# Kernel optimization log

Measured on AMD Instinct MI355X. Metric: run time of the kernel, lower is better.

## Reference

```python
import jax, jax.numpy as jnp
import numpy as np

D, B, T, d = 4, 512, 64, 256  # num_dof, batch, seq_length, per-dof state dim


def setup_inputs() -> dict:
    key = jax.random.key(0)
    ks = jax.random.split(key, 17)
    w = lambda k, s: jax.random.normal(k, s, dtype=jnp.float32) * 0.05
    return {
        "x": jax.random.normal(ks[0], (D, B, T, d), dtype=jnp.float32),
        "wu": w(ks[1], (D, 2 * d, d)), "wf": w(ks[2], (D, 2 * d, d)),
        "wo": w(ks[3], (D, 2 * d, d)), "wc": w(ks[4], (D, 2 * d, d)),
        "bu": w(ks[5], (D, d)), "bf": w(ks[6], (D, d)),
        "bo": w(ks[7], (D, d)), "bc": w(ks[8], (D, d)),
        "gwu": w(ks[9], (D, D * d, d)), "gwf": w(ks[10], (D, D * d, d)),
        "gwo": w(ks[11], (D, D * d, d)), "gwc": w(ks[12], (D, D * d, d)),
        "gbu": w(ks[13], (D, d)), "gbf": w(ks[14], (D, d)),
        "gbo": w(ks[15], (D, d)), "gbc": w(ks[16], (D, d)),
    }


def reference(x, wu, wf, wo, wc, bu, bf, bo, bc,
              gwu, gwf, gwo, gwc, gbu, gbf, gbo, gbc):
    # x: [D, B, T, d]  (dof-stacked inputs_list)
    nD, nB, nT, nd = x.shape
    h0 = jnp.zeros((nD, nB, nd), x.dtype)
    m0 = jnp.zeros((nD, nB, nd), x.dtype)
    xt = jnp.transpose(x, (2, 0, 1, 3))  # [T, D, B, d]

    def step(carry, x_t):
        h, m = carry  # each [D, B, d]
        # --- per-dof LSTM cell (dofs independent here) ---
        inp = jnp.concatenate([x_t, h], axis=-1)  # [D, B, 2d]
        gu = jax.nn.sigmoid(jnp.einsum('dbi,dij->dbj', inp, wu) + bu[:, None, :])
        gf = jax.nn.sigmoid(jnp.einsum('dbi,dij->dbj', inp, wf) + bf[:, None, :])
        go = jax.nn.sigmoid(jnp.einsum('dbi,dij->dbj', inp, wo) + bo[:, None, :])
        gc = jnp.tanh(jnp.einsum('dbi,dij->dbj', inp, wc) + bc[:, None, :])
        m = gf * m + gu * gc
        h = jnp.tanh(go * m)
        # --- grid coupling step: hgrid = concat over dofs ---
        hg = jnp.transpose(h, (1, 0, 2)).reshape(nB, nD * nd)  # [B, D*d]
        gu2 = jax.nn.sigmoid(jnp.einsum('bs,dsj->dbj', hg, gwu) + gbu[:, None, :])
        gf2 = jax.nn.sigmoid(jnp.einsum('bs,dsj->dbj', hg, gwf) + gbf[:, None, :])
        go2 = jax.nn.sigmoid(jnp.einsum('bs,dsj->dbj', hg, gwo) + gbo[:, None, :])
        gc2 = jnp.tanh(jnp.einsum('bs,dsj->dbj', hg, gwc) + gbc[:, None, :])
        m = gf2 * m + gu2 * gc2
        h = jnp.tanh(go2 * m)
        return (h, m), None

    (h, m), _ = jax.lax.scan(step, (h0, m0), xt)
    # stacked [2, D, B, d]: [0]=h_list, [1]=m_list (dof along axis 1)
    return jnp.stack([h, m])
```

## Files before the change

kernel.cpp:

```cpp
#include <hip/hip_runtime.h>
#include <math.h>

#define NDOF 4
#define NB   512
#define NT   64
#define ND   256
#define NS   1024

#define GRID 256

typedef __attribute__((ext_vector_type(8))) __bf16 bf16x8;
typedef __attribute__((ext_vector_type(4))) float  f32x4;

__device__ __forceinline__ void gll16(const void* g, void* l) {
    __builtin_amdgcn_global_load_lds(
        (const __attribute__((address_space(1))) unsigned int*)g,
        (__attribute__((address_space(3))) unsigned int*)l, 16, 0, 0);
}

__device__ __forceinline__ float sig_(float x) { return 1.0f / (1.0f + __expf(-x)); }
__device__ __forceinline__ float tanh_(float x) {
    float e = __expf(-2.0f * fabsf(x));
    float t = (1.0f - e) / (1.0f + e);
    return copysignf(t, x);
}

__device__ __forceinline__ void store16_dev(__bf16* p, bf16x8 v) {
    asm volatile("global_store_dwordx4 %0, %1, off sc0 sc1" :: "v"(p), "v"(v) : "memory");
}
__device__ __forceinline__ void store_flag(unsigned* p, unsigned v) {
    asm volatile("global_store_dword %0, %1, off sc0 sc1" :: "v"(p), "v"(v) : "memory");
}
__device__ __forceinline__ unsigned flag_load(const unsigned* p) {
    unsigned v;
    asm volatile("global_load_dword %0, %1, off sc0 sc1\n\ts_waitcnt vmcnt(0)"
                 : "=v"(v) : "v"(p) : "memory");
    return v;
}

__device__ __forceinline__ void waitv0() {
    asm volatile("s_waitcnt vmcnt(0)" ::: "memory");
    __builtin_amdgcn_sched_barrier(0);
}
__device__ __forceinline__ void waitv8() {
    asm volatile("s_waitcnt vmcnt(8)" ::: "memory");
    __builtin_amdgcn_sched_barrier(0);
}
__device__ __forceinline__ void waitv12() {
    asm volatile("s_waitcnt vmcnt(12)" ::: "memory");
    __builtin_amdgcn_sched_barrier(0);
}

__device__ __forceinline__ void block_bar() {
    __builtin_amdgcn_sched_barrier(0);
    asm volatile("s_waitcnt lgkmcnt(0)\n\ts_barrier" ::: "memory");
    __builtin_amdgcn_sched_barrier(0);
}

__device__ __forceinline__ void poll_flags(const unsigned* f, int nf, unsigned e, int lane) {
    unsigned spins = 0;
    for (;;) {
        unsigned v = e;
        if (lane < nf) v = flag_load(f + lane);
        if (__all(v >= e)) break;
        __builtin_amdgcn_s_sleep(1);
        if (++spins > (1u << 15)) break;
    }
}

struct Params {
    const __bf16* xbf;
    const __bf16* wT1;
    const __bf16* wT2;
    const float *b1u, *b1f, *b1o, *b1c;
    const float *b2u, *b2f, *b2o, *b2c;
    const __bf16* hInit;
    __bf16* ring;
    float*  out;
    unsigned* flags;
};

__device__ __forceinline__ void issueB(bf16x8* smem, const __bf16* wrow,
                                       int pair, int rot, int mask, int tid) {
    const int rowB = tid & 127;
    const int kgb  = (tid >> 7) & 1;
    const int bb = 2048 + (pair & 3) * 1024;
    const int k0 = ((pair + rot) & mask) * 64;
    #pragma unroll
    for (int i = 0; i < 4; ++i) {
        const int kg = kgb + 2 * i;
        gll16(wrow + k0 + kg * 8, &smem[bb + kg * 128 + rowB]);
    }
}
template<int XIT>
__device__ __forceinline__ void issueA(bf16x8* smem, const __bf16* ax,
                                       const __bf16* ah, int pair, int rot, int mask,
                                       int tid) {
    const int rowA = tid & 63;
    const int kga  = tid >> 6;
    const int bb = (pair & 3) * 512;
    const __bf16* base;
    if (XIT > 0 && pair < XIT) base = ax + (size_t)rowA * ND + pair * 64;
    else base = ah + (size_t)rowA * NS + (((pair + rot) & mask) * 64 - XIT * 64);
    #pragma unroll
    for (int i = 0; i < 2; ++i) {
        const int kg = kga + 4 * i;
        gll16(base + kg * 8, &smem[bb + kg * 64 + rowA]);
    }
}

template<int NIT, int XIT>
__device__ __forceinline__ void gemm_seg(bf16x8* smem,
    const __bf16* ax, const __bf16* ah, const __bf16* wrow, int rot,
    const unsigned* gateF, int gateN, unsigned gateE,
    f32x4 (&acc)[2][4], int lane, int wr, int ws, int tid)
{
    constexpr int NSEG = NIT / 2;
    #pragma unroll 1
    for (int s = 0; s < NSEG; ++s) {
        waitv0();
        block_bar();
        if (s == 1 && gateF != nullptr) {
            if (tid < 64) poll_flags(gateF, gateN, gateE, lane);
            block_bar();
        }
        if (s + 1 < NSEG) {
            issueB(smem, wrow, 2 * s + 2, rot, NIT - 1, tid);
            issueB(smem, wrow, 2 * s + 3, rot, NIT - 1, tid);
            issueA<XIT>(smem, ax, ah, 2 * s + 2, rot, NIT - 1, tid);
            issueA<XIT>(smem, ax, ah, 2 * s + 3, rot, NIT - 1, tid);
        }
        #pragma unroll
        for (int q = 0; q < 2; ++q) {
            const int bbA = ((2 * s + q) & 3) * 512;
            const int bbB = 2048 + ((2 * s + q) & 3) * 1024;
            #pragma unroll
            for (int sub = 0; sub < 2; ++sub) {
                const int kq = sub * 4 + (lane >> 4);
                bf16x8 a[2], b[4];
                #pragma unroll
                for (int mI = 0; mI < 2; ++mI)
                    a[mI] = smem[bbA + kq * 64 + wr + mI * 16 + (lane & 15)];
                #pragma unroll
                for (int g = 0; g < 4; ++g)
                    b[g] = smem[bbB + kq * 128 + g * 32 + ws * 16 + (lane & 15)];
                #pragma unroll
                for (int mI = 0; mI < 2; ++mI)
                    #pragma unroll
                    for (int g = 0; g < 4; ++g)
                        acc[mI][g] = __builtin_amdgcn_mfma_f32_16x16x32_bf16(a[mI], b[g], acc[mI][g], 0, 0, 0);
            }
        }
    }
}

__device__ __forceinline__ void epi_stage(const f32x4 (&acc)[2][4], float (&m_reg)[8],
    float bu, float bf_, float bo, float bc,
    char* stg, int wrL, int colq)
{
    #pragma unroll
    for (int mI = 0; mI < 2; ++mI) {
        #pragma unroll
        for (int r = 0; r < 4; ++r) {
            const int rowL = wrL + mI * 16 + r;
            const float gu = sig_(acc[mI][0][r] + bu);
            const float gf = sig_(acc[mI][1][r] + bf_);
            const float go = sig_(acc[mI][2][r] + bo);
            const float gc = tanh_(acc[mI][3][r] + bc);
            float& m = m_reg[mI * 4 + r];
            m = gf * m + gu * gc;
            ((__bf16*)(stg + rowL * 80))[colq] = (__bf16)tanh_(go * m);
        }
    }
}

__device__ __forceinline__ void flush_h(char* stg, __bf16* hbase, int r0,
                                        int scolBase, int tid)
{
    const int rowL = tid >> 2;
    const int off  = tid & 3;
    bf16x8 v = *(bf16x8*)(stg + rowL * 80 + off * 16);
    store16_dev(hbase + (size_t)(r0 + rowL) * NS + scolBase + off * 8, v);
}

__device__ __forceinline__ void epi_last(const f32x4 (&acc)[2][4], float (&m_reg)[8],
    float bu, float bf_, float bo, float bc,
    char* hs, char* ms, int wrL, int colq)
{
    #pragma unroll
    for (int mI = 0; mI < 2; ++mI) {
        #pragma unroll
        for (int r = 0; r < 4; ++r) {
            const int rowL = wrL + mI * 16 + r;
            const float gu = sig_(acc[mI][0][r] + bu);
            const float gf = sig_(acc[mI][1][r] + bf_);
            const float go = sig_(acc[mI][2][r] + bo);
            const float gc = tanh_(acc[mI][3][r] + bc);
            float& m = m_reg[mI * 4 + r];
            m = gf * m + gu * gc;
            ((float*)(hs + rowL * 144))[colq] = tanh_(go * m);
            ((float*)(ms + rowL * 144))[colq] = m;
        }
    }
}

__global__ __launch_bounds__(256, 1)
void lstm_persistent(Params p)
{
    __shared__ bf16x8 smem[6464];
    char* stg = (char*)&smem[6144];

    const int tid  = threadIdx.x;
    const int lane = tid & 63;
    const int wv   = tid >> 6;
    const int wr   = (wv >> 1) * 32;
    const int ws   = wv & 1;

    const int xcd   = blockIdx.x & 7;
    const int local = blockIdx.x >> 3;
    const int dof   = xcd & 3;
    const int rt    = (xcd >> 2) * 4 + (local >> 3);
    const int strip = local & 7;
    const int c0    = strip * 32;
    const int r0    = rt * 64;
    const int grp   = rt * 4 + dof;

    const int colq = ws * 16 + (lane & 15);
    const int scol = dof * ND + c0 + colq;
    const int scolBase = dof * ND + c0;
    const int wrL  = wr + (lane >> 4) * 4;

    const int rowB = tid & 127;
    const int npT  = dof * 1024 + (rowB >> 5) * 256 + c0 + (rowB & 31);
    const __bf16* wrow1 = p.wT1 + (size_t)npT * 512;
    const __bf16* wrow2 = p.wT2 + (size_t)npT * 1024;

    const float b1u = p.b1u[scol], b1f = p.b1f[scol], b1o = p.b1o[scol], b1c = p.b1c[scol];
    const float b2u = p.b2u[scol], b2f = p.b2f[scol], b2o = p.b2o[scol], b2c = p.b2c[scol];

    float m_reg[8];
    #pragma unroll
    for (int i = 0; i < 8; ++i) m_reg[i] = 0.f;

    unsigned* fP1own = p.flags + grp * 8;
    unsigned* fP1rt  = p.flags + rt * 32;
    unsigned* fP2own = p.flags + 256 + grp * 8;
    unsigned* myP1   = p.flags + grp * 8 + strip;
    unsigned* myP2   = p.flags + 256 + grp * 8 + strip;
    const int rot2 = dof * 4;

    auto slot = [&](int i) -> __bf16* { return p.ring + ((size_t)i << 19); };

    {
        const __bf16* ax0 = p.xbf + ((size_t)(dof * NT) * NB + r0) * ND;
        issueB(smem, wrow1, 0, 0, 7, tid);
        issueB(smem, wrow1, 1, 0, 7, tid);
        issueA<4>(smem, ax0, nullptr, 0, 0, 7, tid);
        issueA<4>(smem, ax0, nullptr, 1, 0, 7, tid);
    }

    #pragma unroll 1
    for (int t = 0; t < NT; ++t) {
        const __bf16* ax  = p.xbf + ((size_t)(dof * NT + t) * NB + r0) * ND;
        const __bf16* ah1 = (t == 0 ? p.hInit : slot(2 * t - 1)) + (size_t)r0 * NS + dof * ND;
        __bf16* h1out = slot(2 * t);
        const __bf16* ah2 = slot(2 * t) + (size_t)r0 * NS;
        __bf16* h2out = slot(2 * t + 1);

        f32x4 acc[2][4];
        #pragma unroll
        for (int mI = 0; mI < 2; ++mI)
            #pragma unroll
            for (int g = 0; g < 4; ++g) acc[mI][g] = (f32x4){0.f, 0.f, 0.f, 0.f};

        gemm_seg<8, 4>(smem, ax, ah1, wrow1, 0, fP2own, 8, (unsigned)t,
                       acc, lane, wr, ws, tid);

        epi_stage(acc, m_reg, b1u, b1f, b1o, b1c, stg, wrL, colq);
        block_bar();
        flush_h(stg, h1out, r0, scolBase, tid);
        issueB(smem, wrow2, 0, rot2, 15, tid);
        issueB(smem, wrow2, 1, rot2, 15, tid);
        waitv8();
        block_bar();
        if (tid == 0) store_flag(myP1, (unsigned)(t + 1));
        if (tid < 64) poll_flags(fP1own, 8, (unsigned)(t + 1), lane);
        block_bar();
        issueA<0>(smem, nullptr, ah2, 0, rot2, 15, tid);
        issueA<0>(smem, nullptr, ah2, 1, rot2, 15, tid);

        #pragma unroll
        for (int mI = 0; mI < 2; ++mI)
            #pragma unroll
            for (int g = 0; g < 4; ++g) acc[mI][g] = (f32x4){0.f, 0.f, 0.f, 0.f};

        gemm_seg<16, 0>(smem, nullptr, ah2, wrow2, rot2, fP1rt, 32, (unsigned)(t + 1),
                        acc, lane, wr, ws, tid);

        if (t + 1 < NT) {
            epi_stage(acc, m_reg, b2u, b2f, b2o, b2c, stg, wrL, colq);
            block_bar();
            flush_h(stg, h2out, r0, scolBase, tid);
            const __bf16* axn = p.xbf + ((size_t)(dof * NT + t + 1) * NB + r0) * ND;
            issueB(smem, wrow1, 0, 0, 7, tid);
            issueB(smem, wrow1, 1, 0, 7, tid);
            issueA<4>(smem, axn, nullptr, 0, 0, 7, tid);
            issueA<4>(smem, axn, nullptr, 1, 0, 7, tid);
            waitv12();
            block_bar();
            if (tid == 0) store_flag(myP2, (unsigned)(t + 1));
        } else {
            block_bar();
            char* hs = (char*)smem;
            char* ms = (char*)smem + 9216;
            epi_last(acc, m_reg, b2u, b2f, b2o, b2c, hs, ms, wrL, colq);
            block_bar();
            #pragma unroll
            for (int k = 0; k < 2; ++k) {
                const int c = tid + 256 * k;
                const int rowL = c >> 3;
                const int off  = c & 7;
                const size_t gi = ((size_t)dof * NB + r0 + rowL) * ND + c0 + off * 4;
                *(f32x4*)(p.out + gi) = *(f32x4*)(hs + rowL * 144 + off * 16);
                *(f32x4*)(p.out + (size_t)NDOF * NB * ND + gi) = *(f32x4*)(ms + rowL * 144 + off * 16);
            }
        }
    }
}

__global__ __launch_bounds__(256)
void convert_x(const float* __restrict__ x, __bf16* __restrict__ xbf)
{
    const int id  = blockIdx.x * 256 + threadIdx.x;
    const int d0  = (id & 31) * 8;
    const int t   = (id >> 5) & 63;
    const int b   = (id >> 11) & 511;
    const int dof = id >> 20;
    const float* s = x + (((size_t)dof * NB + b) * NT + t) * ND + d0;
    const float4 v0 = *(const float4*)s;
    const float4 v1 = *(const float4*)(s + 4);
    bf16x8 o;
    o[0] = (__bf16)v0.x; o[1] = (__bf16)v0.y; o[2] = (__bf16)v0.z; o[3] = (__bf16)v0.w;
    o[4] = (__bf16)v1.x; o[5] = (__bf16)v1.y; o[6] = (__bf16)v1.z; o[7] = (__bf16)v1.w;
    *(bf16x8*)(xbf + (((size_t)dof * NT + t) * NB + b) * ND + d0) = o;
}

__global__ __launch_bounds__(256)
void transpose_weights(const float* __restrict__ wu, const float* __restrict__ wf,
                       const float* __restrict__ wo, const float* __restrict__ wcp,
                       const float* __restrict__ gwu, const float* __restrict__ gwf,
                       const float* __restrict__ gwo, const float* __restrict__ gwc,
                       __bf16* __restrict__ wT1, __bf16* __restrict__ wT2)
{
    int id = blockIdx.x * 256 + threadIdx.x;
    const int C1 = 4096 * 64;
    int K, np, kc;
    const float *s0, *s1, *s2, *s3;
    __bf16* dst;
    if (id < C1) { K = 512;  np = id & 4095; kc = id >> 12; dst = wT1; s0 = wu;  s1 = wf;  s2 = wo;  s3 = wcp; }
    else { id -= C1; K = 1024; np = id & 4095; kc = id >> 12; dst = wT2; s0 = gwu; s1 = gwf; s2 = gwo; s3 = gwc; }
    const int dof = np >> 10, q = np & 1023, g = q >> 8, col = q & 255;
    const float* w = ((g == 0) ? s0 : (g == 1) ? s1 : (g == 2) ? s2 : s3)
                     + ((size_t)dof * K + kc * 8) * ND + col;
    bf16x8 o;
    #pragma unroll
    for (int j = 0; j < 8; ++j) o[j] = (__bf16)w[j * ND];
    *(bf16x8*)(dst + (size_t)np * K + kc * 8) = o;
}

extern "C" void kernel_launch(void* const* d_in, const int* in_sizes, int n_in,
                              void* d_out, int out_size, void* d_ws, size_t ws_size,
                              hipStream_t stream)
{
    const float* x   = (const float*)d_in[0];
    const float* wu  = (const float*)d_in[1];
    const float* wf  = (const float*)d_in[2];
    const float* wo  = (const float*)d_in[3];
    const float* wc  = (const float*)d_in[4];

    char* ws = (char*)d_ws;
    __bf16* wT1  = (__bf16*)ws;
    __bf16* wT2  = (__bf16*)(ws + (4u  << 20));
    __bf16* xbf  = (__bf16*)(ws + (12u << 20));
    __bf16* hIn  = (__bf16*)(ws + (76u << 20));
    unsigned* flags = (unsigned*)(ws + (78u << 20));
    __bf16* ring = (__bf16*)(ws + (80u << 20));

    convert_x<<<16384, 256, 0, stream>>>(x, xbf);
    transpose_weights<<<3072, 256, 0, stream>>>(
        wu, wf, wo, wc,
        (const float*)d_in[9], (const float*)d_in[10],
        (const float*)d_in[11], (const float*)d_in[12], wT1, wT2);
    hipMemsetAsync(ws + (76u << 20), 0, (2u << 20) + 8192, stream);

    Params p;
    p.xbf = xbf; p.wT1 = wT1; p.wT2 = wT2;
    p.b1u = (const float*)d_in[5];  p.b1f = (const float*)d_in[6];
    p.b1o = (const float*)d_in[7];  p.b1c = (const float*)d_in[8];
    p.b2u = (const float*)d_in[13]; p.b2f = (const float*)d_in[14];
    p.b2o = (const float*)d_in[15]; p.b2c = (const float*)d_in[16];
    p.hInit = hIn; p.ring = ring; p.out = (float*)d_out; p.flags = flags;

    lstm_persistent<<<dim3(GRID), dim3(256), 0, stream>>>(p);
}
```

Measured before the change: 1.568 ms.

## Double persistent grid to 512 blocks with 16-column strips per block

```diff
diff --git a/kernel.cpp b/kernel.cpp
--- a/kernel.cpp
+++ b/kernel.cpp
@@ -7,10 +7,11 @@
 #define ND   256
 #define NS   1024
 
-#define GRID 256
+#define GRID 512
 
 typedef __attribute__((ext_vector_type(8))) __bf16 bf16x8;
 typedef __attribute__((ext_vector_type(4))) float  f32x4;
+typedef __attribute__((ext_vector_type(2))) unsigned u32x2;
 
 __device__ __forceinline__ void gll16(const void* g, void* l) {
     __builtin_amdgcn_global_load_lds(
@@ -25,8 +26,8 @@
     return copysignf(t, x);
 }
 
-__device__ __forceinline__ void store16_dev(__bf16* p, bf16x8 v) {
-    asm volatile("global_store_dwordx4 %0, %1, off sc0 sc1" :: "v"(p), "v"(v) : "memory");
+__device__ __forceinline__ void store8_dev(__bf16* p, u32x2 v) {
+    asm volatile("global_store_dwordx2 %0, %1, off sc0 sc1" :: "v"(p), "v"(v) : "memory");
 }
 __device__ __forceinline__ void store_flag(unsigned* p, unsigned v) {
     asm volatile("global_store_dword %0, %1, off sc0 sc1" :: "v"(p), "v"(v) : "memory");
@@ -42,12 +43,12 @@
     asm volatile("s_waitcnt vmcnt(0)" ::: "memory");
     __builtin_amdgcn_sched_barrier(0);
 }
+__device__ __forceinline__ void waitv4() {
+    asm volatile("s_waitcnt vmcnt(4)" ::: "memory");
+    __builtin_amdgcn_sched_barrier(0);
+}
 __device__ __forceinline__ void waitv8() {
     asm volatile("s_waitcnt vmcnt(8)" ::: "memory");
-    __builtin_amdgcn_sched_barrier(0);
-}
-__device__ __forceinline__ void waitv12() {
-    asm volatile("s_waitcnt vmcnt(12)" ::: "memory");
     __builtin_amdgcn_sched_barrier(0);
 }
 
@@ -82,38 +83,31 @@
 
 __device__ __forceinline__ void issueB(bf16x8* smem, const __bf16* wrow,
                                        int pair, int rot, int mask, int tid) {
-    const int rowB = tid & 127;
-    const int kgb  = (tid >> 7) & 1;
-    const int bb = 2048 + (pair & 3) * 1024;
+    const int bb = 2048 + (pair & 3) * 512;
     const int k0 = ((pair + rot) & mask) * 64;
-    #pragma unroll
-    for (int i = 0; i < 4; ++i) {
-        const int kg = kgb + 2 * i;
-        gll16(wrow + k0 + kg * 8, &smem[bb + kg * 128 + rowB]);
-    }
+    const int koff = (tid >> 6) * 8;
+    gll16(wrow + k0 + koff,      &smem[bb + tid]);
+    gll16(wrow + k0 + koff + 32, &smem[bb + 256 + tid]);
 }
 template<int XIT>
 __device__ __forceinline__ void issueA(bf16x8* smem, const __bf16* ax,
                                        const __bf16* ah, int pair, int rot, int mask,
                                        int tid) {
+    const int bb = (pair & 3) * 512;
     const int rowA = tid & 63;
-    const int kga  = tid >> 6;
-    const int bb = (pair & 3) * 512;
+    const int koff = (tid >> 6) * 8;
     const __bf16* base;
     if (XIT > 0 && pair < XIT) base = ax + (size_t)rowA * ND + pair * 64;
     else base = ah + (size_t)rowA * NS + (((pair + rot) & mask) * 64 - XIT * 64);
-    #pragma unroll
-    for (int i = 0; i < 2; ++i) {
-        const int kg = kga + 4 * i;
-        gll16(base + kg * 8, &smem[bb + kg * 64 + rowA]);
-    }
+    gll16(base + koff,      &smem[bb + tid]);
+    gll16(base + koff + 32, &smem[bb + 256 + tid]);
 }
 
 template<int NIT, int XIT>
 __device__ __forceinline__ void gemm_seg(bf16x8* smem,
     const __bf16* ax, const __bf16* ah, const __bf16* wrow, int rot,
     const unsigned* gateF, int gateN, unsigned gateE,
-    f32x4 (&acc)[2][4], int lane, int wr, int ws, int tid)
+    f32x4 (&acc)[4], int lane, int wr, int tid)
 {
     constexpr int NSEG = NIT / 2;
     #pragma unroll 1
@@ -133,44 +127,37 @@
         #pragma unroll
         for (int q = 0; q < 2; ++q) {
             const int bbA = ((2 * s + q) & 3) * 512;
-            const int bbB = 2048 + ((2 * s + q) & 3) * 1024;
+            const int bbB = 2048 + ((2 * s + q) & 3) * 512;
             #pragma unroll
             for (int sub = 0; sub < 2; ++sub) {
                 const int kq = sub * 4 + (lane >> 4);
-                bf16x8 a[2], b[4];
-                #pragma unroll
-                for (int mI = 0; mI < 2; ++mI)
-                    a[mI] = smem[bbA + kq * 64 + wr + mI * 16 + (lane & 15)];
+                bf16x8 a = smem[bbA + kq * 64 + wr + (lane & 15)];
+                bf16x8 b[4];
                 #pragma unroll
                 for (int g = 0; g < 4; ++g)
-                    b[g] = smem[bbB + kq * 128 + g * 32 + ws * 16 + (lane & 15)];
+                    b[g] = smem[bbB + kq * 64 + g * 16 + (lane & 15)];
                 #pragma unroll
-                for (int mI = 0; mI < 2; ++mI)
-                    #pragma unroll
-                    for (int g = 0; g < 4; ++g)
-                        acc[mI][g] = __builtin_amdgcn_mfma_f32_16x16x32_bf16(a[mI], b[g], acc[mI][g], 0, 0, 0);
+                for (int g = 0; g < 4; ++g)
+                    acc[g] = __builtin_amdgcn_mfma_f32_16x16x32_bf16(a, b[g], acc[g], 0, 0, 0);
             }
         }
     }
 }
 
-__device__ __forceinline__ void epi_stage(const f32x4 (&acc)[2][4], float (&m_reg)[8],
+__device__ __forceinline__ void epi_stage(const f32x4 (&acc)[4], float (&m_reg)[4],
     float bu, float bf_, float bo, float bc,
     char* stg, int wrL, int colq)
 {
     #pragma unroll
-    for (int mI = 0; mI < 2; ++mI) {
-        #pragma unroll
-        for (int r = 0; r < 4; ++r) {
-            const int rowL = wrL + mI * 16 + r;
-            const float gu = sig_(acc[mI][0][r] + bu);
-            const float gf = sig_(acc[mI][1][r] + bf_);
-            const float go = sig_(acc[mI][2][r] + bo);
-            const float gc = tanh_(acc[mI][3][r] + bc);
-            float& m = m_reg[mI * 4 + r];
-            m = gf * m + gu * gc;
-            ((__bf16*)(stg + rowL * 80))[colq] = (__bf16)tanh_(go * m);
-        }
+    for (int r = 0; r < 4; ++r) {
+        const int rowL = wrL + r;
+        const float gu = sig_(acc[0][r] + bu);
+        const float gf = sig_(acc[1][r] + bf_);
+        const float go = sig_(acc[2][r] + bo);
+        const float gc = tanh_(acc[3][r] + bc);
+        float& m = m_reg[r];
+        m = gf * m + gu * gc;
+        ((__bf16*)(stg + rowL * 48))[colq] = (__bf16)tanh_(go * m);
     }
 }
 
@@ -179,74 +166,70 @@
 {
     const int rowL = tid >> 2;
     const int off  = tid & 3;
-    bf16x8 v = *(bf16x8*)(stg + rowL * 80 + off * 16);
-    store16_dev(hbase + (size_t)(r0 + rowL) * NS + scolBase + off * 8, v);
-}
-
-__device__ __forceinline__ void epi_last(const f32x4 (&acc)[2][4], float (&m_reg)[8],
+    u32x2 v = *(const u32x2*)(stg + rowL * 48 + off * 8);
+    store8_dev(hbase + (size_t)(r0 + rowL) * NS + scolBase + off * 4, v);
+}
+
+__device__ __forceinline__ void epi_last(const f32x4 (&acc)[4], float (&m_reg)[4],
     float bu, float bf_, float bo, float bc,
     char* hs, char* ms, int wrL, int colq)
 {
     #pragma unroll
-    for (int mI = 0; mI < 2; ++mI) {
-        #pragma unroll
-        for (int r = 0; r < 4; ++r) {
-            const int rowL = wrL + mI * 16 + r;
-            const float gu = sig_(acc[mI][0][r] + bu);
-            const float gf = sig_(acc[mI][1][r] + bf_);
-            const float go = sig_(acc[mI][2][r] + bo);
-            const float gc = tanh_(acc[mI][3][r] + bc);
-            float& m = m_reg[mI * 4 + r];
-            m = gf * m + gu * gc;
-            ((float*)(hs + rowL * 144))[colq] = tanh_(go * m);
-            ((float*)(ms + rowL * 144))[colq] = m;
-        }
-    }
-}
-
-__global__ __launch_bounds__(256, 1)
+    for (int r = 0; r < 4; ++r) {
+        const int rowL = wrL + r;
+        const float gu = sig_(acc[0][r] + bu);
+        const float gf = sig_(acc[1][r] + bf_);
+        const float go = sig_(acc[2][r] + bo);
+        const float gc = tanh_(acc[3][r] + bc);
+        float& m = m_reg[r];
+        m = gf * m + gu * gc;
+        ((float*)(hs + rowL * 80))[colq] = tanh_(go * m);
+        ((float*)(ms + rowL * 80))[colq] = m;
+    }
+}
+
+__global__ __launch_bounds__(256, 2)
 void lstm_persistent(Params p)
 {
-    __shared__ bf16x8 smem[6464];
-    char* stg = (char*)&smem[6144];
+    __shared__ bf16x8 smem[4288];
+    char* stg = (char*)&smem[4096];
 
     const int tid  = threadIdx.x;
     const int lane = tid & 63;
     const int wv   = tid >> 6;
-    const int wr   = (wv >> 1) * 32;
-    const int ws   = wv & 1;
+    const int wr   = wv * 16;
 
     const int xcd   = blockIdx.x & 7;
     const int local = blockIdx.x >> 3;
     const int dof   = xcd & 3;
-    const int rt    = (xcd >> 2) * 4 + (local >> 3);
-    const int strip = local & 7;
-    const int c0    = strip * 32;
+    const int rt    = (xcd >> 2) * 4 + (local >> 4);
+    const int strip = local & 15;
+    const int c0    = strip * 16;
     const int r0    = rt * 64;
     const int grp   = rt * 4 + dof;
 
-    const int colq = ws * 16 + (lane & 15);
+    const int colq = lane & 15;
     const int scol = dof * ND + c0 + colq;
     const int scolBase = dof * ND + c0;
     const int wrL  = wr + (lane >> 4) * 4;
 
-    const int rowB = tid & 127;
-    const int npT  = dof * 1024 + (rowB >> 5) * 256 + c0 + (rowB & 31);
+    const int q63 = tid & 63;
+    const int npT = dof * 1024 + (q63 >> 4) * 256 + c0 + (q63 & 15);
     const __bf16* wrow1 = p.wT1 + (size_t)npT * 512;
     const __bf16* wrow2 = p.wT2 + (size_t)npT * 1024;
 
     const float b1u = p.b1u[scol], b1f = p.b1f[scol], b1o = p.b1o[scol], b1c = p.b1c[scol];
     const float b2u = p.b2u[scol], b2f = p.b2f[scol], b2o = p.b2o[scol], b2c = p.b2c[scol];
 
-    float m_reg[8];
+    float m_reg[4];
     #pragma unroll
-    for (int i = 0; i < 8; ++i) m_reg[i] = 0.f;
-
-    unsigned* fP1own = p.flags + grp * 8;
-    unsigned* fP1rt  = p.flags + rt * 32;
-    unsigned* fP2own = p.flags + 256 + grp * 8;
-    unsigned* myP1   = p.flags + grp * 8 + strip;
-    unsigned* myP2   = p.flags + 256 + grp * 8 + strip;
+    for (int i = 0; i < 4; ++i) m_reg[i] = 0.f;
+
+    unsigned* fP1own = p.flags + grp * 16;
+    unsigned* fP1rt  = p.flags + rt * 64;
+    unsigned* fP2own = p.flags + 512 + grp * 16;
+    unsigned* myP1   = p.flags + grp * 16 + strip;
+    unsigned* myP2   = p.flags + 512 + grp * 16 + strip;
     const int rot2 = dof * 4;
 
     auto slot = [&](int i) -> __bf16* { return p.ring + ((size_t)i << 19); };
@@ -267,35 +250,31 @@
         const __bf16* ah2 = slot(2 * t) + (size_t)r0 * NS;
         __bf16* h2out = slot(2 * t + 1);
 
-        f32x4 acc[2][4];
+        f32x4 acc[4];
         #pragma unroll
-        for (int mI = 0; mI < 2; ++mI)
-            #pragma unroll
-            for (int g = 0; g < 4; ++g) acc[mI][g] = (f32x4){0.f, 0.f, 0.f, 0.f};
-
-        gemm_seg<8, 4>(smem, ax, ah1, wrow1, 0, fP2own, 8, (unsigned)t,
-                       acc, lane, wr, ws, tid);
+        for (int g = 0; g < 4; ++g) acc[g] = (f32x4){0.f, 0.f, 0.f, 0.f};
+
+        gemm_seg<8, 4>(smem, ax, ah1, wrow1, 0, fP2own, 16, (unsigned)t,
+                       acc, lane, wr, tid);
 
         epi_stage(acc, m_reg, b1u, b1f, b1o, b1c, stg, wrL, colq);
         block_bar();
         flush_h(stg, h1out, r0, scolBase, tid);
         issueB(smem, wrow2, 0, rot2, 15, tid);
         issueB(smem, wrow2, 1, rot2, 15, tid);
-        waitv8();
+        waitv4();
         block_bar();
         if (tid == 0) store_flag(myP1, (unsigned)(t + 1));
-        if (tid < 64) poll_flags(fP1own, 8, (unsigned)(t + 1), lane);
+        if (tid < 64) poll_flags(fP1own, 16, (unsigned)(t + 1), lane);
         block_bar();
         issueA<0>(smem, nullptr, ah2, 0, rot2, 15, tid);
         issueA<0>(smem, nullptr, ah2, 1, rot2, 15, tid);
 
         #pragma unroll
-        for (int mI = 0; mI < 2; ++mI)
-            #pragma unroll
-            for (int g = 0; g < 4; ++g) acc[mI][g] = (f32x4){0.f, 0.f, 0.f, 0.f};
-
-        gemm_seg<16, 0>(smem, nullptr, ah2, wrow2, rot2, fP1rt, 32, (unsigned)(t + 1),
-                        acc, lane, wr, ws, tid);
+        for (int g = 0; g < 4; ++g) acc[g] = (f32x4){0.f, 0.f, 0.f, 0.f};
+
+        gemm_seg<16, 0>(smem, nullptr, ah2, wrow2, rot2, fP1rt, 64, (unsigned)(t + 1),
+                        acc, lane, wr, tid);
 
         if (t + 1 < NT) {
             epi_stage(acc, m_reg, b2u, b2f, b2o, b2c, stg, wrL, colq);
@@ -306,24 +285,20 @@
             issueB(smem, wrow1, 1, 0, 7, tid);
             issueA<4>(smem, axn, nullptr, 0, 0, 7, tid);
             issueA<4>(smem, axn, nullptr, 1, 0, 7, tid);
-            waitv12();
+            waitv8();
             block_bar();
             if (tid == 0) store_flag(myP2, (unsigned)(t + 1));
         } else {
             block_bar();
             char* hs = (char*)smem;
-            char* ms = (char*)smem + 9216;
+            char* ms = (char*)smem + 5120;
             epi_last(acc, m_reg, b2u, b2f, b2o, b2c, hs, ms, wrL, colq);
             block_bar();
-            #pragma unroll
-            for (int k = 0; k < 2; ++k) {
-                const int c = tid + 256 * k;
-                const int rowL = c >> 3;
-                const int off  = c & 7;
-                const size_t gi = ((size_t)dof * NB + r0 + rowL) * ND + c0 + off * 4;
-                *(f32x4*)(p.out + gi) = *(f32x4*)(hs + rowL * 144 + off * 16);
-                *(f32x4*)(p.out + (size_t)NDOF * NB * ND + gi) = *(f32x4*)(ms + rowL * 144 + off * 16);
-            }
+            const int rowL = tid >> 2;
+            const int off  = tid & 3;
+            const size_t gi = ((size_t)dof * NB + r0 + rowL) * ND + c0 + off * 4;
+            *(f32x4*)(p.out + gi) = *(f32x4*)(hs + rowL * 80 + off * 16);
+            *(f32x4*)(p.out + (size_t)NDOF * NB * ND + gi) = *(f32x4*)(ms + rowL * 80 + off * 16);
         }
     }
 }
```

After: 1.821 ms. +16.1%, slower.
